# Optimization experiments

Hardware: AMD Instinct MI355X
Metric: run time of the kernel (lower is better)

Reference implementation:

```python
import jax, jax.numpy as jnp
import numpy as np

# Model hyperparameters (match init_kwargs)
G = 256      # graph_size
K = 6        # conv kernel size
CH = 8       # channels
ROWS = 4
COLS = 3
B = 64       # batch
H = G - K + 1  # conv output side (square) = 251


def setup_inputs() -> dict:
    key = jax.random.key(0)
    k1, k2, k3, k4 = jax.random.split(key, 4)
    x = jax.random.normal(k1, (B, G, G), dtype=jnp.float32)
    # Conv2d(1, CH, (K,K)) weights, kaiming_normal_ (fan_in = 1*K*K, gain=sqrt(2))
    fan_in = 1 * K * K
    conv_w = jax.random.normal(k2, (CH, 1, K, K), dtype=jnp.float32) * np.float32(np.sqrt(2.0 / fan_in))
    # torch Conv2d default bias init: U(-1/sqrt(fan_in), 1/sqrt(fan_in))
    bound = np.float32(1.0 / np.sqrt(fan_in))
    conv_b = jax.random.uniform(k3, (CH,), dtype=jnp.float32, minval=-bound, maxval=bound)
    # coef parameter [CH, ROWS, COLS], kaiming_normal_ (fan_in = ROWS*COLS)
    coef = jax.random.normal(k4, (CH, ROWS, COLS), dtype=jnp.float32) * np.float32(np.sqrt(2.0 / (ROWS * COLS)))
    return {"x": x, "conv_w": conv_w, "conv_b": conv_b, "coef": coef}


def _traces_of_powers(C):
    """C: [H,H]. Returns traces of C^(i+2) for i in 0..ROWS-1 (matches torch loop:
    x_series[0]=C@C; at step i it records trace(x_series[i]) = trace(C^(i+2))."""
    def step(P, _):
        return C @ P, jnp.trace(P)
    _, ts = jax.lax.scan(step, C @ C, None, length=ROWS)
    return ts  # [ROWS]


def reference(x, conv_w, conv_b, coef):
    # conv over each sample treated as [1,1,G,G] -> vectorized as [B,1,G,G]
    y = jax.lax.conv_general_dilated(
        x[:, None], conv_w, window_strides=(1, 1), padding='VALID',
        dimension_numbers=('NCHW', 'OIHW', 'NCHW'))
    y = y + conv_b[None, :, None, None]           # [B, CH, H, H]

    ts = jax.vmap(jax.vmap(_traces_of_powers))(y)  # [B, CH, ROWS]

    jpow = jnp.arange(1, COLS + 1, dtype=jnp.float32)            # exponents j+1
    ret = ts[..., None] ** jpow                                  # [B, CH, ROWS, COLS]
    numel = jnp.float32(H * H)
    exps = (jnp.arange(ROWS, dtype=jnp.float32)[:, None]
            + jnp.arange(COLS, dtype=jnp.float32)[None, :] + 1.0)  # i+j+1
    ret = ret / (numel ** exps)                                  # [B, CH, ROWS, COLS]

    terms = coef[None] * ret
    return terms.sum(axis=(1, 2, 3))  # [B]
```

## Files before the change

### kernel.cpp

```cpp
#include <hip/hip_runtime.h>

typedef short short8 __attribute__((ext_vector_type(8)));
typedef float f32x4 __attribute__((ext_vector_type(4)));

#define B_    64
#define CH_   8
#define NBC   512
#define MATU  65536
#define H_    251
#define PADX  73
#define LDSW  40

__device__ inline unsigned short bf16r(float f){
    unsigned u = __float_as_uint(f);
    u += 0x7fffu + ((u >> 16) & 1u);
    return (unsigned short)(u >> 16);
}
__device__ inline float bf16f(unsigned short h){ return __uint_as_float(((unsigned)h) << 16); }
__device__ inline unsigned packsplit(float v){
    unsigned short h = bf16r(v);
    unsigned short l = bf16r(v - bf16f(h));
    return (((unsigned)h) << 16) | (unsigned)l;
}
__device__ inline float unpackf(unsigned u){
    return __uint_as_float(u & 0xffff0000u) + bf16f((unsigned short)(u & 0xffffu));
}

__global__ __launch_bounds__(256) void conv_pack(const float* __restrict__ x,
                                                 const float* __restrict__ w,
                                                 const float* __restrict__ bias,
                                                 unsigned* __restrict__ Ypk,
                                                 int b_base) {
    __shared__ float xt[69 * PADX];
    __shared__ float wsm[148];

    int tid = threadIdx.x;
    int tile = blockIdx.x;
    int lb = blockIdx.y;
    int cq = blockIdx.z;
    int b = b_base + lb;
    int r0 = (tile >> 2) * 64, c0 = (tile & 3) * 64;

    if (tid < 144) wsm[tid] = w[cq * 144 + tid];
    if (tid < 4)   wsm[144 + tid] = bias[cq * 4 + tid];

    const float* xb = x + (size_t)b * 65536;
    for (int idx = tid; idx < 69 * PADX; idx += 256) {
        int row = idx / PADX, col = idx - row * PADX;
        float v = 0.f;
        if (col < 69) {
            int gr = r0 + row; if (gr > 255) gr = 255;
            int gc = c0 + col; if (gc > 255) gc = 255;
            v = xb[gr * 256 + gc];
        }
        xt[idx] = v;
    }
    __syncthreads();

    int tx = tid & 15, ty = tid >> 4;

    float acc[4][4][4];
    #pragma unroll
    for (int cc = 0; cc < 4; ++cc) {
        float bv = wsm[144 + cc];
        #pragma unroll
        for (int i = 0; i < 4; ++i)
            #pragma unroll
            for (int j = 0; j < 4; ++j) acc[cc][i][j] = bv;
    }

    #pragma unroll
    for (int ir = 0; ir < 9; ++ir) {
        float row[9];
        #pragma unroll
        for (int c = 0; c < 9; ++c) row[c] = xt[(ty * 4 + ir) * PADX + tx * 4 + c];
        #pragma unroll
        for (int cc = 0; cc < 4; ++cc) {
            const float* wc = &wsm[cc * 36];
            #pragma unroll
            for (int i = 0; i < 4; ++i) {
                int u = ir - i;
                if (u >= 0 && u < 6) {
                    #pragma unroll
                    for (int v = 0; v < 6; ++v) {
                        float wv = wc[u * 6 + v];
                        #pragma unroll
                        for (int j = 0; j < 4; ++j) acc[cc][i][j] += row[j + v] * wv;
                    }
                }
            }
        }
    }

    #pragma unroll
    for (int cc = 0; cc < 4; ++cc) {
        int ch = cq * 4 + cc;
        unsigned pk[4][4];
        #pragma unroll
        for (int i = 0; i < 4; ++i) {
            int gr = r0 + ty * 4 + i;
            #pragma unroll
            for (int j = 0; j < 4; ++j) {
                int gc = c0 + tx * 4 + j;
                float v = (gr < H_ && gc < H_) ? acc[cc][i][j] : 0.f;
                pk[i][j] = packsplit(v);
            }
        }
        unsigned* yrow = Ypk + (size_t)(lb * 8 + ch) * MATU;
        #pragma unroll
        for (int i = 0; i < 4; ++i) {
            uint4 v = make_uint4(pk[i][0], pk[i][1], pk[i][2], pk[i][3]);
            *(uint4*)&yrow[(size_t)(r0 + ty * 4 + i) * 256 + c0 + tx * 4] = v;
        }
    }
}

template<int PHASE>
__global__ __launch_bounds__(256) void gemm_mfma(const unsigned* __restrict__ Apk,
                                                 const unsigned* __restrict__ Ypk,
                                                 unsigned* __restrict__ Mpk,
                                                 double* __restrict__ pdiag,
                                                 double* __restrict__ pfull,
                                                 int bc_base, int cur) {
    __shared__ __align__(16) char smem[53248];
    __shared__ double redbuf[8];

    unsigned short* Ahi = (unsigned short*)smem;
    unsigned short* Alo = (unsigned short*)(smem + 10240);
    unsigned short* Bhi = (unsigned short*)(smem + 20480);
    unsigned short* Blo = (unsigned short*)(smem + 36864);

    int tid = threadIdx.x;

    int hw = blockIdx.x;
    int xcd = hw & 7, s = hw >> 3;
    int mpx = cur >> 3;
    int lbc = xcd * mpx + (s >> 2);
    int t4 = s & 3;
    int by = t4 >> 1, bx = t4 & 1;
    int bi = by * 128, bj = bx * 128;
    int bc = bc_base + lbc;

    const unsigned* A = Apk + (size_t)lbc * MATU;

    int wid = tid >> 6, l = tid & 63;
    int wr = wid >> 1, wc = wid & 1;
    int l15 = l & 15, lk = l >> 4;

    f32x4 acc[4][4];
    #pragma unroll
    for (int m = 0; m < 4; ++m)
        #pragma unroll
        for (int n = 0; n < 4; ++n) acc[m][n] = (f32x4){0.f, 0.f, 0.f, 0.f};

    const int cl  = tid & 31;
    const int grp = tid >> 5;
    const int kq  = grp * 4;
    const int kb  = grp >> 1;
    const int koff = (grp & 1) * 4;

    for (int k0 = 0; k0 < 256; k0 += 32) {
        #pragma unroll
        for (int p = 0; p < 4; ++p) {
            int g = p * 256 + tid;
            int row = g >> 3, chn = g & 7;
            uint4 qa = *(const uint4*)(A + (size_t)(bi + row) * 256 + k0 + chn * 4);
            *(ushort4*)&Ahi[row * LDSW + chn * 4] =
                make_ushort4(qa.x >> 16, qa.y >> 16, qa.z >> 16, qa.w >> 16);
            *(ushort4*)&Alo[row * LDSW + chn * 4] =
                make_ushort4(qa.x & 0xffff, qa.y & 0xffff, qa.z & 0xffff, qa.w & 0xffff);
        }
        {
            const unsigned* Bp = A + (size_t)(k0 + kq) * 256 + bj + cl;
            unsigned d[4][4];
            #pragma unroll
            for (int i = 0; i < 4; ++i)
                #pragma unroll
                for (int j = 0; j < 4; ++j)
                    d[i][j] = Bp[i * 256 + j * 32];
            #pragma unroll
            for (int j = 0; j < 4; ++j) {
                int c = cl + 32 * j;
                *(ushort4*)&Bhi[kb * 1024 + c * 8 + koff] =
                    make_ushort4(d[0][j] >> 16, d[1][j] >> 16, d[2][j] >> 16, d[3][j] >> 16);
                *(ushort4*)&Blo[kb * 1024 + c * 8 + koff] =
                    make_ushort4(d[0][j] & 0xffff, d[1][j] & 0xffff, d[2][j] & 0xffff, d[3][j] & 0xffff);
            }
        }
        __syncthreads();

        short8 ah[4], al[4], bh[4], bl[4];
        #pragma unroll
        for (int m = 0; m < 4; ++m) {
            int r = wr * 64 + m * 16 + l15;
            ah[m] = *(const short8*)&Ahi[r * LDSW + lk * 8];
            al[m] = *(const short8*)&Alo[r * LDSW + lk * 8];
        }
        #pragma unroll
        for (int n = 0; n < 4; ++n) {
            int c = wc * 64 + n * 16 + l15;
            bh[n] = *(const short8*)&Bhi[lk * 1024 + c * 8];
            bl[n] = *(const short8*)&Blo[lk * 1024 + c * 8];
        }
        #pragma unroll
        for (int m = 0; m < 4; ++m)
            #pragma unroll
            for (int n = 0; n < 4; ++n) {
                acc[m][n] = __builtin_amdgcn_mfma_f32_16x16x32_bf16(ah[m], bh[n], acc[m][n], 0, 0, 0);
                acc[m][n] = __builtin_amdgcn_mfma_f32_16x16x32_bf16(ah[m], bl[n], acc[m][n], 0, 0, 0);
                acc[m][n] = __builtin_amdgcn_mfma_f32_16x16x32_bf16(al[m], bh[n], acc[m][n], 0, 0, 0);
            }
        __syncthreads();
    }

    const unsigned* Yb = Ypk + (size_t)lbc * MATU;
    unsigned* Mw = (PHASE == 1) ? (Mpk + (size_t)lbc * MATU) : nullptr;
    float s_full = 0.f, s_diag = 0.f;
    #pragma unroll
    for (int m = 0; m < 4; ++m) {
        int rg0 = bi + wr * 64 + m * 16 + lk * 4;
        #pragma unroll
        for (int n = 0; n < 4; ++n) {
            int cg = bj + wc * 64 + n * 16 + l15;
            uint4 yq = *(const uint4*)(Yb + (size_t)cg * 256 + rg0);
            unsigned yu[4] = {yq.x, yq.y, yq.z, yq.w};
            f32x4 v = acc[m][n];
            #pragma unroll
            for (int reg = 0; reg < 4; ++reg) {
                float val = v[reg];
                s_full += val * unpackf(yu[reg]);
                if (rg0 + reg == cg) s_diag += val;
                if (PHASE == 1) Mw[(size_t)(rg0 + reg) * 256 + cg] = packsplit(val);
            }
        }
    }

    double df = (double)s_full, dd = (double)s_diag;
    #pragma unroll
    for (int off = 32; off > 0; off >>= 1) {
        df += __shfl_down(df, off, 64);
        dd += __shfl_down(dd, off, 64);
    }
    __syncthreads();
    if (l == 0) { redbuf[wid] = df; redbuf[4 + wid] = dd; }
    __syncthreads();
    if (tid == 0) {
        pfull[(size_t)bc * 4 + by * 2 + bx] =
            redbuf[0] + redbuf[1] + redbuf[2] + redbuf[3];
        if (bx == by)
            pdiag[(size_t)bc * 2 + bx] =
                redbuf[4] + redbuf[5] + redbuf[6] + redbuf[7];
    }
}

__global__ void combine(const double* __restrict__ p2, const double* __restrict__ p3,
                        const double* __restrict__ p4, const double* __restrict__ p5,
                        const float* __restrict__ coef, float* __restrict__ out) {
    int b = threadIdx.x;
    if (b >= B_) return;
    const double numel = (double)(H_ * H_);
    double acc = 0.0;
    for (int ch = 0; ch < CH_; ++ch) {
        int bc = b * CH_ + ch;
        double t[4];
        t[0] = p2[bc * 2] + p2[bc * 2 + 1];
        t[1] = p3[bc * 4] + p3[bc * 4 + 1] + p3[bc * 4 + 2] + p3[bc * 4 + 3];
        t[2] = p4[bc * 2] + p4[bc * 2 + 1];
        t[3] = p5[bc * 4] + p5[bc * 4 + 1] + p5[bc * 4 + 2] + p5[bc * 4 + 3];
        double npow_i = numel;
        for (int i = 0; i < 4; ++i) {
            double tv = t[i];
            double p = tv, d = npow_i;
            for (int j = 0; j < 3; ++j) {
                acc += (double)coef[ch * 12 + i * 3 + j] * (p / d);
                p *= tv;
                d *= numel;
            }
            npow_i *= numel;
        }
    }
    out[b] = (float)acc;
}

extern "C" void kernel_launch(void* const* d_in, const int* in_sizes, int n_in,
                              void* d_out, int out_size, void* d_ws, size_t ws_size,
                              hipStream_t stream) {
    const float* x    = (const float*)d_in[0];
    const float* w    = (const float*)d_in[1];
    const float* bias = (const float*)d_in[2];
    const float* coef = (const float*)d_in[3];
    float* out = (float*)d_out;

    double* p2 = (double*)d_ws;
    double* p3 = p2 + NBC * 2;
    double* p4 = p3 + NBC * 4;
    double* p5 = p4 + NBC * 2;
    const size_t head = 65536;

    const size_t per_mat = (size_t)MATU * 4;
    size_t avail = (ws_size > head) ? ws_size - head : 0;
    int NC = (int)(avail / (2 * per_mat));
    NC &= ~7;
    if (NC > 256) NC = 256;
    if (NC < 8) NC = 8;

    unsigned* Ypk = (unsigned*)((char*)d_ws + head);
    unsigned* Mpk = Ypk + (size_t)NC * MATU;

    for (int bc0 = 0; bc0 < NBC; bc0 += NC) {
        int cur = NBC - bc0;
        if (cur > NC) cur = NC;
        int nb = cur / 8;
        conv_pack<<<dim3(16, nb, 2), 256, 0, stream>>>(x, w, bias, Ypk, bc0 / 8);
        gemm_mfma<1><<<cur * 4, 256, 0, stream>>>(Ypk, Ypk, Mpk, p2, p3, bc0, cur);
        gemm_mfma<2><<<cur * 4, 256, 0, stream>>>(Mpk, Ypk, nullptr, p4, p5, bc0, cur);
    }
    combine<<<1, 64, 0, stream>>>(p2, p3, p4, p5, coef, out);
}
```

Baseline: 253.4 us.

## Store split-bf16 matrices as separate hi/lo planes and write transposed M

```diff
diff --git a/kernel.cpp b/kernel.cpp
--- a/kernel.cpp
+++ b/kernel.cpp
@@ -6,7 +6,7 @@
 #define B_    64
 #define CH_   8
 #define NBC   512
-#define MATU  65536
+#define MATE  65536
 #define H_    251
 #define PADX  73
 #define LDSW  40
@@ -17,19 +17,12 @@
     return (unsigned short)(u >> 16);
 }
 __device__ inline float bf16f(unsigned short h){ return __uint_as_float(((unsigned)h) << 16); }
-__device__ inline unsigned packsplit(float v){
-    unsigned short h = bf16r(v);
-    unsigned short l = bf16r(v - bf16f(h));
-    return (((unsigned)h) << 16) | (unsigned)l;
-}
-__device__ inline float unpackf(unsigned u){
-    return __uint_as_float(u & 0xffff0000u) + bf16f((unsigned short)(u & 0xffffu));
-}
 
 __global__ __launch_bounds__(256) void conv_pack(const float* __restrict__ x,
                                                  const float* __restrict__ w,
                                                  const float* __restrict__ bias,
-                                                 unsigned* __restrict__ Ypk,
+                                                 unsigned short* __restrict__ Yhi,
+                                                 unsigned short* __restrict__ Ylo,
                                                  int b_base) {
     __shared__ float xt[69 * PADX];
     __shared__ float wsm[148];
@@ -95,40 +88,41 @@
     #pragma unroll
     for (int cc = 0; cc < 4; ++cc) {
         int ch = cq * 4 + cc;
-        unsigned pk[4][4];
+        size_t mb = (size_t)(lb * 8 + ch) * MATE;
         #pragma unroll
         for (int i = 0; i < 4; ++i) {
             int gr = r0 + ty * 4 + i;
+            unsigned short h4[4], l4[4];
             #pragma unroll
             for (int j = 0; j < 4; ++j) {
                 int gc = c0 + tx * 4 + j;
                 float v = (gr < H_ && gc < H_) ? acc[cc][i][j] : 0.f;
-                pk[i][j] = packsplit(v);
-            }
-        }
-        unsigned* yrow = Ypk + (size_t)(lb * 8 + ch) * MATU;
-        #pragma unroll
-        for (int i = 0; i < 4; ++i) {
-            uint4 v = make_uint4(pk[i][0], pk[i][1], pk[i][2], pk[i][3]);
-            *(uint4*)&yrow[(size_t)(r0 + ty * 4 + i) * 256 + c0 + tx * 4] = v;
+                unsigned short h = bf16r(v);
+                h4[j] = h;
+                l4[j] = bf16r(v - bf16f(h));
+            }
+            size_t off = mb + (size_t)gr * 256 + c0 + tx * 4;
+            *(ushort4*)(Yhi + off) = make_ushort4(h4[0], h4[1], h4[2], h4[3]);
+            *(ushort4*)(Ylo + off) = make_ushort4(l4[0], l4[1], l4[2], l4[3]);
         }
     }
 }
 
 template<int PHASE>
-__global__ __launch_bounds__(256) void gemm_mfma(const unsigned* __restrict__ Apk,
-                                                 const unsigned* __restrict__ Ypk,
-                                                 unsigned* __restrict__ Mpk,
+__global__ __launch_bounds__(256) void gemm_mfma(const unsigned short* __restrict__ Xhi,
+                                                 const unsigned short* __restrict__ Xlo,
+                                                 const unsigned short* __restrict__ Yehi,
+                                                 const unsigned short* __restrict__ Yelo,
+                                                 unsigned short* __restrict__ MTohi,
+                                                 unsigned short* __restrict__ MTolo,
                                                  double* __restrict__ pdiag,
                                                  double* __restrict__ pfull,
                                                  int bc_base, int cur) {
-    __shared__ __align__(16) char smem[53248];
+    __shared__ __align__(16) unsigned short Ahi[128 * LDSW];
+    __shared__ __align__(16) unsigned short Alo[128 * LDSW];
+    __shared__ __align__(16) unsigned short Bhi[128 * LDSW];
+    __shared__ __align__(16) unsigned short Blo[128 * LDSW];
     __shared__ double redbuf[8];
-
-    unsigned short* Ahi = (unsigned short*)smem;
-    unsigned short* Alo = (unsigned short*)(smem + 10240);
-    unsigned short* Bhi = (unsigned short*)(smem + 20480);
-    unsigned short* Blo = (unsigned short*)(smem + 36864);
 
     int tid = threadIdx.x;
 
@@ -141,7 +135,8 @@
     int bi = by * 128, bj = bx * 128;
     int bc = bc_base + lbc;
 
-    const unsigned* A = Apk + (size_t)lbc * MATU;
+    const unsigned short* Xh = Xhi + (size_t)lbc * MATE;
+    const unsigned short* Xl = Xlo + (size_t)lbc * MATE;
 
     int wid = tid >> 6, l = tid & 63;
     int wr = wid >> 1, wc = wid & 1;
@@ -153,39 +148,46 @@
         #pragma unroll
         for (int n = 0; n < 4; ++n) acc[m][n] = (f32x4){0.f, 0.f, 0.f, 0.f};
 
-    const int cl  = tid & 31;
-    const int grp = tid >> 5;
-    const int kq  = grp * 4;
-    const int kb  = grp >> 1;
-    const int koff = (grp & 1) * 4;
+    const int cp = tid & 63;
+    const int kc = tid >> 6;
+
+    const int linbase = (PHASE == 1) ? bi : bj;
+    const int trbase  = (PHASE == 1) ? bj : bi;
+    unsigned short* LinHi = (PHASE == 1) ? Ahi : Bhi;
+    unsigned short* LinLo = (PHASE == 1) ? Alo : Blo;
+    unsigned short* TrHi  = (PHASE == 1) ? Bhi : Ahi;
+    unsigned short* TrLo  = (PHASE == 1) ? Blo : Alo;
 
     for (int k0 = 0; k0 < 256; k0 += 32) {
         #pragma unroll
-        for (int p = 0; p < 4; ++p) {
-            int g = p * 256 + tid;
-            int row = g >> 3, chn = g & 7;
-            uint4 qa = *(const uint4*)(A + (size_t)(bi + row) * 256 + k0 + chn * 4);
-            *(ushort4*)&Ahi[row * LDSW + chn * 4] =
-                make_ushort4(qa.x >> 16, qa.y >> 16, qa.z >> 16, qa.w >> 16);
-            *(ushort4*)&Alo[row * LDSW + chn * 4] =
-                make_ushort4(qa.x & 0xffff, qa.y & 0xffff, qa.z & 0xffff, qa.w & 0xffff);
+        for (int p = 0; p < 2; ++p) {
+            int idx = p * 256 + tid;
+            int row = idx >> 2, ch = idx & 3;
+            size_t off = (size_t)(linbase + row) * 256 + k0 + ch * 8;
+            *(uint4*)&LinHi[row * LDSW + ch * 8] = *(const uint4*)(Xh + off);
+            *(uint4*)&LinLo[row * LDSW + ch * 8] = *(const uint4*)(Xl + off);
         }
         {
-            const unsigned* Bp = A + (size_t)(k0 + kq) * 256 + bj + cl;
-            unsigned d[4][4];
-            #pragma unroll
-            for (int i = 0; i < 4; ++i)
-                #pragma unroll
-                for (int j = 0; j < 4; ++j)
-                    d[i][j] = Bp[i * 256 + j * 32];
-            #pragma unroll
-            for (int j = 0; j < 4; ++j) {
-                int c = cl + 32 * j;
-                *(ushort4*)&Bhi[kb * 1024 + c * 8 + koff] =
-                    make_ushort4(d[0][j] >> 16, d[1][j] >> 16, d[2][j] >> 16, d[3][j] >> 16);
-                *(ushort4*)&Blo[kb * 1024 + c * 8 + koff] =
-                    make_ushort4(d[0][j] & 0xffff, d[1][j] & 0xffff, d[2][j] & 0xffff, d[3][j] & 0xffff);
-            }
+            const unsigned short* sh = Xh + (size_t)(k0 + kc * 8) * 256 + trbase + 2 * cp;
+            const unsigned short* sl = Xl + (size_t)(k0 + kc * 8) * 256 + trbase + 2 * cp;
+            unsigned uh[8], ul[8];
+            #pragma unroll
+            for (int kk = 0; kk < 8; ++kk) {
+                uh[kk] = *(const unsigned*)(sh + kk * 256);
+                ul[kk] = *(const unsigned*)(sl + kk * 256);
+            }
+            unsigned e[4], o[4], el[4], ol[4];
+            #pragma unroll
+            for (int q = 0; q < 4; ++q) {
+                e[q]  = (uh[2*q] & 0xffffu) | (uh[2*q+1] << 16);
+                o[q]  = (uh[2*q] >> 16)     | (uh[2*q+1] & 0xffff0000u);
+                el[q] = (ul[2*q] & 0xffffu) | (ul[2*q+1] << 16);
+                ol[q] = (ul[2*q] >> 16)     | (ul[2*q+1] & 0xffff0000u);
+            }
+            *(uint4*)&TrHi[(2*cp)     * LDSW + kc * 8] = make_uint4(e[0], e[1], e[2], e[3]);
+            *(uint4*)&TrHi[(2*cp + 1) * LDSW + kc * 8] = make_uint4(o[0], o[1], o[2], o[3]);
+            *(uint4*)&TrLo[(2*cp)     * LDSW + kc * 8] = make_uint4(el[0], el[1], el[2], el[3]);
+            *(uint4*)&TrLo[(2*cp + 1) * LDSW + kc * 8] = make_uint4(ol[0], ol[1], ol[2], ol[3]);
         }
         __syncthreads();
 
@@ -199,8 +201,8 @@
         #pragma unroll
         for (int n = 0; n < 4; ++n) {
             int c = wc * 64 + n * 16 + l15;
-            bh[n] = *(const short8*)&Bhi[lk * 1024 + c * 8];
-            bl[n] = *(const short8*)&Blo[lk * 1024 + c * 8];
+            bh[n] = *(const short8*)&Bhi[c * LDSW + lk * 8];
+            bl[n] = *(const short8*)&Blo[c * LDSW + lk * 8];
         }
         #pragma unroll
         for (int m = 0; m < 4; ++m)
@@ -213,8 +215,8 @@
         __syncthreads();
     }
 
-    const unsigned* Yb = Ypk + (size_t)lbc * MATU;
-    unsigned* Mw = (PHASE == 1) ? (Mpk + (size_t)lbc * MATU) : nullptr;
+    const unsigned short* Yh = Yehi + (size_t)lbc * MATE;
+    const unsigned short* Yl = Yelo + (size_t)lbc * MATE;
     float s_full = 0.f, s_diag = 0.f;
     #pragma unroll
     for (int m = 0; m < 4; ++m) {
@@ -222,15 +224,28 @@
         #pragma unroll
         for (int n = 0; n < 4; ++n) {
             int cg = bj + wc * 64 + n * 16 + l15;
-            uint4 yq = *(const uint4*)(Yb + (size_t)cg * 256 + rg0);
-            unsigned yu[4] = {yq.x, yq.y, yq.z, yq.w};
+            size_t yoff = (size_t)cg * 256 + rg0;
+            ushort4 yh = *(const ushort4*)(Yh + yoff);
+            ushort4 yl = *(const ushort4*)(Yl + yoff);
+            unsigned short yhv[4] = {yh.x, yh.y, yh.z, yh.w};
+            unsigned short ylv[4] = {yl.x, yl.y, yl.z, yl.w};
             f32x4 v = acc[m][n];
+            unsigned short mh[4], ml[4];
             #pragma unroll
             for (int reg = 0; reg < 4; ++reg) {
                 float val = v[reg];
-                s_full += val * unpackf(yu[reg]);
+                s_full += val * (bf16f(yhv[reg]) + bf16f(ylv[reg]));
                 if (rg0 + reg == cg) s_diag += val;
-                if (PHASE == 1) Mw[(size_t)(rg0 + reg) * 256 + cg] = packsplit(val);
+                if (PHASE == 1) {
+                    unsigned short h = bf16r(val);
+                    mh[reg] = h;
+                    ml[reg] = bf16r(val - bf16f(h));
+                }
+            }
+            if (PHASE == 1) {
+                size_t moff = (size_t)lbc * MATE + (size_t)cg * 256 + rg0;
+                *(ushort4*)(MTohi + moff) = make_ushort4(mh[0], mh[1], mh[2], mh[3]);
+                *(ushort4*)(MTolo + moff) = make_ushort4(ml[0], ml[1], ml[2], ml[3]);
             }
         }
     }
@@ -297,23 +312,25 @@
     double* p5 = p4 + NBC * 2;
     const size_t head = 65536;
 
-    const size_t per_mat = (size_t)MATU * 4;
+    const size_t per_plane = (size_t)MATE * 2;
     size_t avail = (ws_size > head) ? ws_size - head : 0;
-    int NC = (int)(avail / (2 * per_mat));
+    int NC = (int)(avail / (4 * per_plane));
     NC &= ~7;
     if (NC > 256) NC = 256;
     if (NC < 8) NC = 8;
 
-    unsigned* Ypk = (unsigned*)((char*)d_ws + head);
-    unsigned* Mpk = Ypk + (size_t)NC * MATU;
+    unsigned short* Yhi  = (unsigned short*)((char*)d_ws + head);
+    unsigned short* Ylo  = Yhi  + (size_t)NC * MATE;
+    unsigned short* MThi = Ylo  + (size_t)NC * MATE;
+    unsigned short* MTlo = MThi + (size_t)NC * MATE;
 
     for (int bc0 = 0; bc0 < NBC; bc0 += NC) {
         int cur = NBC - bc0;
         if (cur > NC) cur = NC;
         int nb = cur / 8;
-        conv_pack<<<dim3(16, nb, 2), 256, 0, stream>>>(x, w, bias, Ypk, bc0 / 8);
-        gemm_mfma<1><<<cur * 4, 256, 0, stream>>>(Ypk, Ypk, Mpk, p2, p3, bc0, cur);
-        gemm_mfma<2><<<cur * 4, 256, 0, stream>>>(Mpk, Ypk, nullptr, p4, p5, bc0, cur);
+        conv_pack<<<dim3(16, nb, 2), 256, 0, stream>>>(x, w, bias, Yhi, Ylo, bc0 / 8);
+        gemm_mfma<1><<<cur * 4, 256, 0, stream>>>(Yhi, Ylo, Yhi, Ylo, MThi, MTlo, p2, p3, bc0, cur);
+        gemm_mfma<2><<<cur * 4, 256, 0, stream>>>(MThi, MTlo, Yhi, Ylo, nullptr, nullptr, p4, p5, bc0, cur);
     }
     combine<<<1, 64, 0, stream>>>(p2, p3, p4, p5, coef, out);
 }
```

New measurement: 315.5 us. 1.25x slower.
